# Kernel optimization log

Measured on AMD Instinct MI355X. Metric: run time of the kernel, lower is better.

Reference implementation:

```python
import jax, jax.numpy as jnp
import numpy as np

EPS = 1e-7

def setup_inputs() -> dict:
    key = jax.random.key(0)
    k1, k2, k3, k4 = jax.random.split(key, 4)
    B, F, NA = 4096, 512, 8192
    return {
        "x_real": jax.random.normal(k1, (B, F), dtype=jnp.float32),
        "x_imag": jax.random.normal(k2, (B, F), dtype=jnp.float32),
        "att_real": jax.random.normal(k3, (NA, F), dtype=jnp.float32),
        "att_imag": jax.random.normal(k4, (NA, F), dtype=jnp.float32),
        "alpha": jnp.float32(0.2),
        "top_k": 32,
    }

def _l2_normalize(v):
    # faiss.normalize_L2: divide each row by its L2 norm
    return v / jnp.linalg.norm(v, axis=1, keepdims=True)

def reference(x_real, x_imag, att_real, att_imag, alpha, top_k):
    # Database = queries themselves + attention tokens (complex, kept as re/im)
    db_re = jnp.concatenate([x_real, att_real], axis=0)   # [N, F]
    db_im = jnp.concatenate([x_imag, att_imag], axis=0)   # [N, F]
    db_reim = _l2_normalize(jnp.concatenate([db_re, db_im], axis=1))  # [N, 2F]
    q_reim = _l2_normalize(jnp.concatenate([x_real, x_imag], axis=1)) # [B, 2F]
    # IndexFlatIP on L2-normalized vectors = cosine similarity brute-force search
    sims = jnp.einsum('bd,nd->bn', q_reim, db_reim)        # [B, N]
    k = min(top_k, db_reim.shape[0])
    _, nn_idx = jax.lax.top_k(sims, k)                     # [B, K]
    nb_re = db_re[nn_idx]                                  # [B, K, F]
    nb_im = db_im[nn_idx]                                  # [B, K, F]
    # circular (polar) mean aggregation
    rho = jnp.sqrt(nb_re * nb_re + nb_im * nb_im) + EPS    # |z| + eps
    phi = jnp.arctan2(nb_im, nb_re)                        # angle(z)
    mean_rho = rho.mean(axis=1)                            # [B, F]
    mean_phi = jnp.arctan2(jnp.sin(phi).mean(axis=1), jnp.cos(phi).mean(axis=1))
    agg_re = mean_rho * jnp.cos(mean_phi)
    agg_im = mean_rho * jnp.sin(mean_phi)
    a = jnp.clip(alpha, 0.0, 1.0)
    out_re = (1.0 - a) * x_real + a * agg_re
    out_im = (1.0 - a) * x_imag + a * agg_im
    return jnp.stack([out_re, out_im], axis=0)             # [2, B, F]
```

## Files before the change

kernel.cpp:

```cpp
#include <hip/hip_runtime.h>
#include <math.h>

#define BQ   4096
#define FD   512
#define NATT 8192
#define NDB  (BQ + NATT)
#define DD   (2 * FD)
#define KTOP 32
#define EPSF 1e-7f

#define QT   32
#define NT   96
#define NTILES (2048 + 528)

typedef __attribute__((ext_vector_type(8))) short bf16x8;
typedef __attribute__((ext_vector_type(8))) unsigned short u16x8;
typedef __attribute__((ext_vector_type(4))) float f32x4;

__device__ unsigned short g_pk[(size_t)NDB * DD * 2];
__device__ float g_sims[(size_t)BQ * NDB];
__device__ float g_tmax[(size_t)BQ * NT];

__device__ __forceinline__ unsigned fkey(unsigned u) {
    return u ^ (unsigned)(((int)u >> 31) | 0x80000000);
}
__device__ __forceinline__ unsigned short f2bf(float f) {
    unsigned u = __float_as_uint(f);
    return (unsigned short)((u + 0x7FFFu + ((u >> 16) & 1u)) >> 16);
}
__device__ __forceinline__ float bf2f(unsigned short h) {
    return __uint_as_float((unsigned)h << 16);
}
__device__ __forceinline__ float frsq(float x) {
#if __has_builtin(__builtin_amdgcn_rsqf)
    return __builtin_amdgcn_rsqf(x);
#else
    return rsqrtf(x);
#endif
}
__device__ __forceinline__ void gld16(const void* g, void* l) {
    __builtin_amdgcn_global_load_lds(
        (const __attribute__((address_space(1))) void*)g,
        (__attribute__((address_space(3))) void*)l, 16, 0, 0);
}

__global__ __launch_bounds__(256) void normalize_kernel(
        const float* __restrict__ x_real, const float* __restrict__ x_imag,
        const float* __restrict__ att_real, const float* __restrict__ att_imag) {
    int t = threadIdx.x;
    int r = t >> 4;
    int l16 = t & 15;
    int row = blockIdx.x * 16 + r;
    const float *re, *im;
    if (row < BQ) { re = x_real + (size_t)row * FD;          im = x_imag + (size_t)row * FD; }
    else          { re = att_real + (size_t)(row - BQ) * FD; im = att_imag + (size_t)(row - BQ) * FD; }

    float4 vre[8], vim[8];
    float ss = 0.0f;
#pragma unroll
    for (int i = 0; i < 8; ++i) {
        vre[i] = *(const float4*)(re + l16 * 32 + i * 4);
        vim[i] = *(const float4*)(im + l16 * 32 + i * 4);
        ss += vre[i].x * vre[i].x + vre[i].y * vre[i].y + vre[i].z * vre[i].z + vre[i].w * vre[i].w;
        ss += vim[i].x * vim[i].x + vim[i].y * vim[i].y + vim[i].z * vim[i].z + vim[i].w * vim[i].w;
    }
#pragma unroll
    for (int o = 1; o < 16; o <<= 1) ss += __shfl_xor(ss, o);
    float ninv = frsq(ss);

    auto emit = [&](const float4* v, int kchunk) {
        unsigned short hi[32], lo[32];
#pragma unroll
        for (int i = 0; i < 8; ++i) {
            float vals[4] = {v[i].x, v[i].y, v[i].z, v[i].w};
#pragma unroll
            for (int j = 0; j < 4; ++j) {
                float nv = vals[j] * ninv;
                unsigned short h = f2bf(nv);
                hi[i * 4 + j] = h;
                lo[i * 4 + j] = f2bf(nv - bf2f(h));
            }
        }
        size_t cb = ((size_t)((row >> 7) * 32 + kchunk) * 2) * 4096 + (size_t)(row & 127) * 8;
#pragma unroll
        for (int kc = 0; kc < 4; ++kc) {
            *(u16x8*)(g_pk + cb + kc * 1024)        = *(u16x8*)&hi[kc * 8];
            *(u16x8*)(g_pk + cb + 4096 + kc * 1024) = *(u16x8*)&lo[kc * 8];
        }
    };
    emit(vre, l16);
    emit(vim, 16 + l16);
}

__global__ __launch_bounds__(256) void gemm_mfma() {
    __shared__ unsigned short smem[4 * 4096];
    const int t = threadIdx.x;
    const int lane = t & 63, wid = t >> 6;
    const int wr = wid >> 1, wc = wid & 1;
    const int kc = lane >> 4, fr = lane & 15;

    int tid = blockIdx.x;
    int bm, bn; bool mirror = false;
    if (tid < 2048) { bm = tid >> 6; bn = QT + (tid & 63); }
    else {
        int t2 = tid - 2048;
        int r = 0, off = 0;
        while (t2 >= off + (QT - r)) { off += QT - r; ++r; }
        bm = r; bn = r + (t2 - off);
        mirror = (bn != bm);
    }

    f32x4 acc[4][4];
#pragma unroll
    for (int m = 0; m < 4; ++m)
#pragma unroll
        for (int n = 0; n < 4; ++n) acc[m][n] = (f32x4){0.f, 0.f, 0.f, 0.f};

    for (int c = 0; c < 32; ++c) {
        const unsigned short* apk = g_pk + ((size_t)(bm * 32 + c)) * 8192;
        const unsigned short* bpk = g_pk + ((size_t)(bn * 32 + c)) * 8192;
#pragma unroll
        for (int i = 0; i < 4; ++i) {
            int s = t + i * 256;
            gld16(apk + (size_t)s * 8, &smem[s * 8]);
            gld16(bpk + (size_t)s * 8, &smem[8192 + s * 8]);
        }
        __syncthreads();

        bf16x8 ah[4], al[4], bh[4], bl[4];
#pragma unroll
        for (int m = 0; m < 4; ++m) {
            int ra = wr * 64 + m * 16 + fr;
            ah[m] = *(const bf16x8*)&smem[(kc * 128 + ra) * 8];
            al[m] = *(const bf16x8*)&smem[4096 + (kc * 128 + ra) * 8];
            int rb = wc * 64 + m * 16 + fr;
            bh[m] = *(const bf16x8*)&smem[8192 + (kc * 128 + rb) * 8];
            bl[m] = *(const bf16x8*)&smem[12288 + (kc * 128 + rb) * 8];
        }
#pragma unroll
        for (int m = 0; m < 4; ++m)
#pragma unroll
            for (int n = 0; n < 4; ++n) {
                acc[m][n] = __builtin_amdgcn_mfma_f32_16x16x32_bf16(ah[m], bh[n], acc[m][n], 0, 0, 0);
                acc[m][n] = __builtin_amdgcn_mfma_f32_16x16x32_bf16(ah[m], bl[n], acc[m][n], 0, 0, 0);
                acc[m][n] = __builtin_amdgcn_mfma_f32_16x16x32_bf16(al[m], bh[n], acc[m][n], 0, 0, 0);
            }
        __syncthreads();
    }
    const int crow0 = bm * 128 + wr * 64 + kc * 4;
    const int ccol0 = bn * 128 + wc * 64 + fr;
#pragma unroll
    for (int m = 0; m < 4; ++m)
#pragma unroll
        for (int n = 0; n < 4; ++n)
#pragma unroll
            for (int j = 0; j < 4; ++j)
                g_sims[(size_t)(crow0 + m * 16 + j) * NDB + ccol0 + n * 16] = acc[m][n][j];

    if (mirror) {
#pragma unroll
        for (int m = 0; m < 4; ++m)
#pragma unroll
            for (int n = 0; n < 4; ++n) {
                size_t r = (size_t)(bn * 128 + wc * 64 + n * 16 + fr);
                size_t cix = (size_t)(bm * 128 + wr * 64 + m * 16 + kc * 4);
                *(f32x4*)&g_sims[r * NDB + cix] = acc[m][n];
            }
    }

    float* rowhalf = (float*)smem;
    float* colhalf = (float*)smem + 256;
#pragma unroll
    for (int m = 0; m < 4; ++m)
#pragma unroll
        for (int j = 0; j < 4; ++j) {
            float v = fmaxf(fmaxf(acc[m][0][j], acc[m][1][j]),
                            fmaxf(acc[m][2][j], acc[m][3][j]));
#pragma unroll
            for (int o = 1; o < 16; o <<= 1) v = fmaxf(v, __shfl_xor(v, o));
            if (fr == 0) rowhalf[(wr * 64 + m * 16 + kc * 4 + j) * 2 + wc] = v;
        }
    if (mirror) {
#pragma unroll
        for (int n = 0; n < 4; ++n) {
            float v = acc[0][n][0];
#pragma unroll
            for (int m = 0; m < 4; ++m)
#pragma unroll
                for (int j = 0; j < 4; ++j) v = fmaxf(v, acc[m][n][j]);
            v = fmaxf(v, __shfl_xor(v, 16));
            v = fmaxf(v, __shfl_xor(v, 32));
            if (kc == 0) colhalf[(wc * 64 + n * 16 + fr) * 2 + wr] = v;
        }
    }
    __syncthreads();
    if (t < 128) {
        g_tmax[(size_t)(bm * 128 + t) * NT + bn] = fmaxf(rowhalf[t * 2], rowhalf[t * 2 + 1]);
        if (mirror)
            g_tmax[(size_t)(bn * 128 + t) * NT + bm] = fmaxf(colhalf[t * 2], colhalf[t * 2 + 1]);
    }
}

__global__ __launch_bounds__(256) void topk_agg_kernel(
        const float* __restrict__ x_real, const float* __restrict__ x_imag,
        const float* __restrict__ att_real, const float* __restrict__ att_imag,
        const float* __restrict__ alpha_p, float* __restrict__ out) {
    __shared__ float stm[96];
    __shared__ unsigned char tlist[96];
    __shared__ unsigned long long cand[512];
    __shared__ int s_idx[KTOP];
    __shared__ unsigned s_cnt;
    __shared__ int s_ntile;
    __shared__ float s_T;
    __shared__ unsigned long long s_red[4];
    __shared__ unsigned long long s_last;
    int b = blockIdx.x, t = threadIdx.x;
    int wave = t >> 6, lane = t & 63;

    if (t < 96) stm[t] = g_tmax[(size_t)b * NT + t];
    if (t == 0) { s_cnt = 0; s_ntile = 0; }
    __syncthreads();

    if (t < 96) {
        float v = stm[t];
        int cnt = 0;
        for (int i = 0; i < 96; ++i) {
            float o = stm[i];
            cnt += (o > v) || (o == v && i < t);
        }
        if (cnt == KTOP - 1) s_T = v;
    }
    __syncthreads();
    const float T = s_T;

    if (t < 96 && stm[t] >= T) {
        int p = atomicAdd(&s_ntile, 1);
        tlist[p] = (unsigned char)t;
    }
    __syncthreads();
    const int ntile = s_ntile;

    const float* rowp = g_sims + (size_t)b * NDB;
    for (int base = 0; base < ntile; base += 8) {
        int ti = base + (t >> 5);
        if (ti < ntile) {
            int tile = tlist[ti];
            int c4 = (t & 31) * 4;
            float4 v = *(const float4*)(rowp + tile * 128 + c4);
            int gidx = tile * 128 + c4;
            if (v.x >= T) { unsigned p = atomicAdd(&s_cnt, 1u); if (p < 512) cand[p] = ((unsigned long long)fkey(__float_as_uint(v.x)) << 32) | (unsigned)(~(gidx + 0)); }
            if (v.y >= T) { unsigned p = atomicAdd(&s_cnt, 1u); if (p < 512) cand[p] = ((unsigned long long)fkey(__float_as_uint(v.y)) << 32) | (unsigned)(~(gidx + 1)); }
            if (v.z >= T) { unsigned p = atomicAdd(&s_cnt, 1u); if (p < 512) cand[p] = ((unsigned long long)fkey(__float_as_uint(v.z)) << 32) | (unsigned)(~(gidx + 2)); }
            if (v.w >= T) { unsigned p = atomicAdd(&s_cnt, 1u); if (p < 512) cand[p] = ((unsigned long long)fkey(__float_as_uint(v.w)) << 32) | (unsigned)(~(gidx + 3)); }
        }
    }
    __syncthreads();

    int c = (int)s_cnt;
    if (c <= 64) {
        if (wave == 0) {
            unsigned long long vv = (lane < c) ? cand[lane] : 0ull;
#pragma unroll
            for (int k = 2; k <= 64; k <<= 1)
#pragma unroll
                for (int j = k >> 1; j > 0; j >>= 1) {
                    unsigned long long o = __shfl_xor(vv, j);
                    bool lower = (lane & j) == 0;
                    bool desc  = (lane & k) == 0;
                    bool keepmax = (lower == desc);
                    vv = keepmax ? (vv > o ? vv : o) : (vv < o ? vv : o);
                }
            if (lane < KTOP) s_idx[lane] = (int)(~(unsigned)vv);
        }
    } else if (c <= 512) {
        if (wave == 0) {
            for (int it = 0; it < KTOP; ++it) {
                unsigned long long m = 0;
                for (int i = lane; i < c; i += 64) m = cand[i] > m ? cand[i] : m;
#pragma unroll
                for (int o = 32; o > 0; o >>= 1) {
                    unsigned long long x = __shfl_xor(m, o);
                    m = x > m ? x : m;
                }
                if (lane == 0) s_idx[it] = (int)(~(unsigned)m);
                for (int i = lane; i < c; i += 64) if (cand[i] == m) cand[i] = 0;
            }
        }
    } else {
        const float4* row4 = (const float4*)rowp;
        unsigned long long last = ~0ull;
        for (int it = 0; it < KTOP; ++it) {
            unsigned long long m = 0;
            for (int i = 0; i < 12; ++i) {
                float4 v = row4[t + i * 256];
                int base = 4 * (t + i * 256);
                unsigned long long k;
                k = ((unsigned long long)fkey(__float_as_uint(v.x)) << 32) | (unsigned)(~(base + 0)); if (k < last && k > m) m = k;
                k = ((unsigned long long)fkey(__float_as_uint(v.y)) << 32) | (unsigned)(~(base + 1)); if (k < last && k > m) m = k;
                k = ((unsigned long long)fkey(__float_as_uint(v.z)) << 32) | (unsigned)(~(base + 2)); if (k < last && k > m) m = k;
                k = ((unsigned long long)fkey(__float_as_uint(v.w)) << 32) | (unsigned)(~(base + 3)); if (k < last && k > m) m = k;
            }
#pragma unroll
            for (int o = 32; o > 0; o >>= 1) {
                unsigned long long x = __shfl_xor(m, o);
                m = x > m ? x : m;
            }
            if (lane == 0) s_red[wave] = m;
            __syncthreads();
            if (t == 0) {
                unsigned long long w = s_red[0];
#pragma unroll
                for (int i = 1; i < 4; ++i) w = s_red[i] > w ? s_red[i] : w;
                s_idx[it] = (int)(~(unsigned)w);
                s_last = w;
            }
            __syncthreads();
            last = s_last;
        }
    }
    __syncthreads();

    float a = alpha_p[0];
    a = fminf(fmaxf(a, 0.0f), 1.0f);
    int f = 2 * t;
    float sr0 = 0, sc0 = 0, ss0 = 0, sr1 = 0, sc1 = 0, ss1 = 0;
    for (int k = 0; k < KTOP; ++k) {
        int idx = s_idx[k];
        const float *re, *im;
        if (idx < BQ) { re = x_real + (size_t)idx * FD;          im = x_imag + (size_t)idx * FD; }
        else          { re = att_real + (size_t)(idx - BQ) * FD; im = att_imag + (size_t)(idx - BQ) * FD; }
        float2 vr = *(const float2*)(re + f);
        float2 vi = *(const float2*)(im + f);
        float s0 = vr.x * vr.x + vi.x * vi.x;
        if (s0 > 0.0f) {
            float iv = frsq(s0);
            sr0 += s0 * iv; sc0 += vr.x * iv; ss0 += vi.x * iv;
        } else sc0 += 1.0f;
        float s1 = vr.y * vr.y + vi.y * vi.y;
        if (s1 > 0.0f) {
            float iv = frsq(s1);
            sr1 += s1 * iv; sc1 += vr.y * iv; ss1 += vi.y * iv;
        } else sc1 += 1.0f;
    }
    const float inv = 1.0f / KTOP;
    float mr0 = sr0 * inv + EPSF, mc0 = sc0 * inv, ms0 = ss0 * inv;
    float mr1 = sr1 * inv + EPSF, mc1 = sc1 * inv, ms1 = ss1 * inv;
    float q0 = mc0 * mc0 + ms0 * ms0;
    float q1 = mc1 * mc1 + ms1 * ms1;
    float i0 = (q0 > 0.0f) ? frsq(q0) : 0.0f;
    float i1 = (q1 > 0.0f) ? frsq(q1) : 0.0f;
    float c0 = (q0 > 0.0f) ? mc0 * i0 : 1.0f;
    float s0v = ms0 * i0;
    float c1 = (q1 > 0.0f) ? mc1 * i1 : 1.0f;
    float s1v = ms1 * i1;
    size_t obase = (size_t)b * FD + f;
    float2 xr = *(const float2*)(x_real + obase);
    float2 xi = *(const float2*)(x_imag + obase);
    float2 outr = make_float2((1.0f - a) * xr.x + a * (mr0 * c0),
                              (1.0f - a) * xr.y + a * (mr1 * c1));
    float2 outi = make_float2((1.0f - a) * xi.x + a * (mr0 * s0v),
                              (1.0f - a) * xi.y + a * (mr1 * s1v));
    *(float2*)(out + obase) = outr;
    *(float2*)(out + (size_t)BQ * FD + obase) = outi;
}

extern "C" void kernel_launch(void* const* d_in, const int* in_sizes, int n_in,
                              void* d_out, int out_size, void* d_ws, size_t ws_size,
                              hipStream_t stream) {
    const float* x_real   = (const float*)d_in[0];
    const float* x_imag   = (const float*)d_in[1];
    const float* att_real = (const float*)d_in[2];
    const float* att_imag = (const float*)d_in[3];
    const float* alpha    = (const float*)d_in[4];
    float* out = (float*)d_out;

    normalize_kernel<<<NDB / 16, 256, 0, stream>>>(x_real, x_imag, att_real, att_imag);
    gemm_mfma<<<NTILES, 256, 0, stream>>>();
    topk_agg_kernel<<<BQ, 256, 0, stream>>>(x_real, x_imag, att_real, att_imag, alpha, out);
}
```

Measured before the change: 376.1 us.

## Use single bf16 GEMM with fp32 rescoring of near-threshold top-k candidates

Drops the split hi/lo bf16 emulation of fp32, so the similarity GEMM runs one MFMA per tile pair instead of three and loads half the packed data. To keep top-k selection exact, the selection threshold is widened by a margin. Candidates whose bf16 score falls inside that ambiguity band are rescored in fp32 against the original inputs using stored inverse norms. If too many candidates sit near the boundary, a fallback path rescores every candidate. This adds candidate-handling complexity and depends on the margin bounding the bf16 error.

New measurement: 333.0 us. 11.5% less time.

```diff
diff --git a/kernel.cpp b/kernel.cpp
--- a/kernel.cpp
+++ b/kernel.cpp
@@ -8,6 +8,7 @@
 #define DD   (2 * FD)
 #define KTOP 32
 #define EPSF 1e-7f
+#define DEL2 0.004f
 
 #define QT   32
 #define NT   96
@@ -17,19 +18,21 @@
 typedef __attribute__((ext_vector_type(8))) unsigned short u16x8;
 typedef __attribute__((ext_vector_type(4))) float f32x4;
 
-__device__ unsigned short g_pk[(size_t)NDB * DD * 2];
+__device__ unsigned short g_pk[(size_t)NDB * DD];
 __device__ float g_sims[(size_t)BQ * NDB];
 __device__ float g_tmax[(size_t)BQ * NT];
+__device__ float g_ninv[NDB];
 
 __device__ __forceinline__ unsigned fkey(unsigned u) {
     return u ^ (unsigned)(((int)u >> 31) | 0x80000000);
+}
+__device__ __forceinline__ float unfkey(unsigned fk) {
+    unsigned u = (fk & 0x80000000u) ? (fk ^ 0x80000000u) : ~fk;
+    return __uint_as_float(u);
 }
 __device__ __forceinline__ unsigned short f2bf(float f) {
     unsigned u = __float_as_uint(f);
     return (unsigned short)((u + 0x7FFFu + ((u >> 16) & 1u)) >> 16);
-}
-__device__ __forceinline__ float bf2f(unsigned short h) {
-    return __uint_as_float((unsigned)h << 16);
 }
 __device__ __forceinline__ float frsq(float x) {
 #if __has_builtin(__builtin_amdgcn_rsqf)
@@ -67,33 +70,27 @@
 #pragma unroll
     for (int o = 1; o < 16; o <<= 1) ss += __shfl_xor(ss, o);
     float ninv = frsq(ss);
+    if (l16 == 0) g_ninv[row] = ninv;
 
     auto emit = [&](const float4* v, int kchunk) {
-        unsigned short hi[32], lo[32];
+        unsigned short hi[32];
 #pragma unroll
         for (int i = 0; i < 8; ++i) {
             float vals[4] = {v[i].x, v[i].y, v[i].z, v[i].w};
 #pragma unroll
-            for (int j = 0; j < 4; ++j) {
-                float nv = vals[j] * ninv;
-                unsigned short h = f2bf(nv);
-                hi[i * 4 + j] = h;
-                lo[i * 4 + j] = f2bf(nv - bf2f(h));
-            }
-        }
-        size_t cb = ((size_t)((row >> 7) * 32 + kchunk) * 2) * 4096 + (size_t)(row & 127) * 8;
-#pragma unroll
-        for (int kc = 0; kc < 4; ++kc) {
-            *(u16x8*)(g_pk + cb + kc * 1024)        = *(u16x8*)&hi[kc * 8];
-            *(u16x8*)(g_pk + cb + 4096 + kc * 1024) = *(u16x8*)&lo[kc * 8];
-        }
+            for (int j = 0; j < 4; ++j) hi[i * 4 + j] = f2bf(vals[j] * ninv);
+        }
+        size_t cb = ((size_t)((row >> 7) * 32 + kchunk)) * 4096 + (size_t)(row & 127) * 8;
+#pragma unroll
+        for (int kc = 0; kc < 4; ++kc)
+            *(u16x8*)(g_pk + cb + kc * 1024) = *(u16x8*)&hi[kc * 8];
     };
     emit(vre, l16);
     emit(vim, 16 + l16);
 }
 
 __global__ __launch_bounds__(256) void gemm_mfma() {
-    __shared__ unsigned short smem[4 * 4096];
+    __shared__ unsigned short smem[2 * 4096];
     const int t = threadIdx.x;
     const int lane = t & 63, wid = t >> 6;
     const int wr = wid >> 1, wc = wid & 1;
@@ -117,34 +114,29 @@
         for (int n = 0; n < 4; ++n) acc[m][n] = (f32x4){0.f, 0.f, 0.f, 0.f};
 
     for (int c = 0; c < 32; ++c) {
-        const unsigned short* apk = g_pk + ((size_t)(bm * 32 + c)) * 8192;
-        const unsigned short* bpk = g_pk + ((size_t)(bn * 32 + c)) * 8192;
-#pragma unroll
-        for (int i = 0; i < 4; ++i) {
+        const unsigned short* apk = g_pk + ((size_t)(bm * 32 + c)) * 4096;
+        const unsigned short* bpk = g_pk + ((size_t)(bn * 32 + c)) * 4096;
+#pragma unroll
+        for (int i = 0; i < 2; ++i) {
             int s = t + i * 256;
             gld16(apk + (size_t)s * 8, &smem[s * 8]);
-            gld16(bpk + (size_t)s * 8, &smem[8192 + s * 8]);
-        }
-        __syncthreads();
-
-        bf16x8 ah[4], al[4], bh[4], bl[4];
+            gld16(bpk + (size_t)s * 8, &smem[4096 + s * 8]);
+        }
+        __syncthreads();
+
+        bf16x8 ah[4], bh[4];
 #pragma unroll
         for (int m = 0; m < 4; ++m) {
             int ra = wr * 64 + m * 16 + fr;
             ah[m] = *(const bf16x8*)&smem[(kc * 128 + ra) * 8];
-            al[m] = *(const bf16x8*)&smem[4096 + (kc * 128 + ra) * 8];
             int rb = wc * 64 + m * 16 + fr;
-            bh[m] = *(const bf16x8*)&smem[8192 + (kc * 128 + rb) * 8];
-            bl[m] = *(const bf16x8*)&smem[12288 + (kc * 128 + rb) * 8];
+            bh[m] = *(const bf16x8*)&smem[4096 + (kc * 128 + rb) * 8];
         }
 #pragma unroll
         for (int m = 0; m < 4; ++m)
 #pragma unroll
-            for (int n = 0; n < 4; ++n) {
+            for (int n = 0; n < 4; ++n)
                 acc[m][n] = __builtin_amdgcn_mfma_f32_16x16x32_bf16(ah[m], bh[n], acc[m][n], 0, 0, 0);
-                acc[m][n] = __builtin_amdgcn_mfma_f32_16x16x32_bf16(ah[m], bl[n], acc[m][n], 0, 0, 0);
-                acc[m][n] = __builtin_amdgcn_mfma_f32_16x16x32_bf16(al[m], bh[n], acc[m][n], 0, 0, 0);
-            }
         __syncthreads();
     }
     const int crow0 = bm * 128 + wr * 64 + kc * 4;
@@ -207,18 +199,24 @@
         const float* __restrict__ alpha_p, float* __restrict__ out) {
     __shared__ float stm[96];
     __shared__ unsigned char tlist[96];
-    __shared__ unsigned long long cand[512];
+    __shared__ unsigned long long cand[1024];
+    __shared__ unsigned long long skey[64];
+    __shared__ unsigned long long rkey[64];
+    __shared__ int ridx[64];
     __shared__ int s_idx[KTOP];
+    __shared__ float qre[FD], qim[FD];
     __shared__ unsigned s_cnt;
-    __shared__ int s_ntile;
-    __shared__ float s_T;
+    __shared__ int s_ntile, s_S, s_R;
+    __shared__ float s_T, s_V32;
     __shared__ unsigned long long s_red[4];
     __shared__ unsigned long long s_last;
     int b = blockIdx.x, t = threadIdx.x;
     int wave = t >> 6, lane = t & 63;
 
     if (t < 96) stm[t] = g_tmax[(size_t)b * NT + t];
-    if (t == 0) { s_cnt = 0; s_ntile = 0; }
+    if (t < 128) *(float4*)&qre[t * 4] = *(const float4*)(x_real + (size_t)b * FD + t * 4);
+    else         *(float4*)&qim[(t - 128) * 4] = *(const float4*)(x_imag + (size_t)b * FD + (t - 128) * 4);
+    if (t == 0) { s_cnt = 0; s_ntile = 0; s_S = 0; s_R = 0; }
     __syncthreads();
 
     if (t < 96) {
@@ -231,12 +229,9 @@
         if (cnt == KTOP - 1) s_T = v;
     }
     __syncthreads();
-    const float T = s_T;
-
-    if (t < 96 && stm[t] >= T) {
-        int p = atomicAdd(&s_ntile, 1);
-        tlist[p] = (unsigned char)t;
-    }
+    const float Tm = s_T - DEL2;
+
+    if (t < 96 && stm[t] >= Tm) { int p = atomicAdd(&s_ntile, 1); tlist[p] = (unsigned char)t; }
     __syncthreads();
     const int ntile = s_ntile;
 
@@ -248,15 +243,16 @@
             int c4 = (t & 31) * 4;
             float4 v = *(const float4*)(rowp + tile * 128 + c4);
             int gidx = tile * 128 + c4;
-            if (v.x >= T) { unsigned p = atomicAdd(&s_cnt, 1u); if (p < 512) cand[p] = ((unsigned long long)fkey(__float_as_uint(v.x)) << 32) | (unsigned)(~(gidx + 0)); }
-            if (v.y >= T) { unsigned p = atomicAdd(&s_cnt, 1u); if (p < 512) cand[p] = ((unsigned long long)fkey(__float_as_uint(v.y)) << 32) | (unsigned)(~(gidx + 1)); }
-            if (v.z >= T) { unsigned p = atomicAdd(&s_cnt, 1u); if (p < 512) cand[p] = ((unsigned long long)fkey(__float_as_uint(v.z)) << 32) | (unsigned)(~(gidx + 2)); }
-            if (v.w >= T) { unsigned p = atomicAdd(&s_cnt, 1u); if (p < 512) cand[p] = ((unsigned long long)fkey(__float_as_uint(v.w)) << 32) | (unsigned)(~(gidx + 3)); }
-        }
-    }
-    __syncthreads();
-
-    int c = (int)s_cnt;
+            if (v.x >= Tm) { unsigned p = atomicAdd(&s_cnt, 1u); if (p < 1024) cand[p] = ((unsigned long long)fkey(__float_as_uint(v.x)) << 32) | (unsigned)(~(gidx + 0)); }
+            if (v.y >= Tm) { unsigned p = atomicAdd(&s_cnt, 1u); if (p < 1024) cand[p] = ((unsigned long long)fkey(__float_as_uint(v.y)) << 32) | (unsigned)(~(gidx + 1)); }
+            if (v.z >= Tm) { unsigned p = atomicAdd(&s_cnt, 1u); if (p < 1024) cand[p] = ((unsigned long long)fkey(__float_as_uint(v.z)) << 32) | (unsigned)(~(gidx + 2)); }
+            if (v.w >= Tm) { unsigned p = atomicAdd(&s_cnt, 1u); if (p < 1024) cand[p] = ((unsigned long long)fkey(__float_as_uint(v.w)) << 32) | (unsigned)(~(gidx + 3)); }
+        }
+    }
+    __syncthreads();
+    unsigned cnt_raw = s_cnt;
+    int c = (int)cnt_raw; if (c > 1024) c = 1024;
+
     if (c <= 64) {
         if (wave == 0) {
             unsigned long long vv = (lane < c) ? cand[lane] : 0ull;
@@ -270,49 +266,122 @@
                     bool keepmax = (lower == desc);
                     vv = keepmax ? (vv > o ? vv : o) : (vv < o ? vv : o);
                 }
-            if (lane < KTOP) s_idx[lane] = (int)(~(unsigned)vv);
-        }
-    } else if (c <= 512) {
-        if (wave == 0) {
-            for (int it = 0; it < KTOP; ++it) {
-                unsigned long long m = 0;
-                for (int i = lane; i < c; i += 64) m = cand[i] > m ? cand[i] : m;
-#pragma unroll
-                for (int o = 32; o > 0; o >>= 1) {
-                    unsigned long long x = __shfl_xor(m, o);
-                    m = x > m ? x : m;
-                }
-                if (lane == 0) s_idx[it] = (int)(~(unsigned)m);
-                for (int i = lane; i < c; i += 64) if (cand[i] == m) cand[i] = 0;
-            }
-        }
+            skey[lane] = vv;
+        }
+        __syncthreads();
     } else {
-        const float4* row4 = (const float4*)rowp;
         unsigned long long last = ~0ull;
-        for (int it = 0; it < KTOP; ++it) {
+        for (int it = 0; it < 64; ++it) {
             unsigned long long m = 0;
-            for (int i = 0; i < 12; ++i) {
-                float4 v = row4[t + i * 256];
-                int base = 4 * (t + i * 256);
-                unsigned long long k;
-                k = ((unsigned long long)fkey(__float_as_uint(v.x)) << 32) | (unsigned)(~(base + 0)); if (k < last && k > m) m = k;
-                k = ((unsigned long long)fkey(__float_as_uint(v.y)) << 32) | (unsigned)(~(base + 1)); if (k < last && k > m) m = k;
-                k = ((unsigned long long)fkey(__float_as_uint(v.z)) << 32) | (unsigned)(~(base + 2)); if (k < last && k > m) m = k;
-                k = ((unsigned long long)fkey(__float_as_uint(v.w)) << 32) | (unsigned)(~(base + 3)); if (k < last && k > m) m = k;
-            }
-#pragma unroll
-            for (int o = 32; o > 0; o >>= 1) {
-                unsigned long long x = __shfl_xor(m, o);
-                m = x > m ? x : m;
-            }
+            for (int i = t; i < c; i += 256) { unsigned long long k = cand[i]; if (k < last && k > m) m = k; }
+#pragma unroll
+            for (int o = 32; o > 0; o >>= 1) { unsigned long long x = __shfl_xor(m, o); m = x > m ? x : m; }
             if (lane == 0) s_red[wave] = m;
             __syncthreads();
             if (t == 0) {
                 unsigned long long w = s_red[0];
 #pragma unroll
                 for (int i = 1; i < 4; ++i) w = s_red[i] > w ? s_red[i] : w;
-                s_idx[it] = (int)(~(unsigned)w);
-                s_last = w;
+                skey[it] = w; s_last = w;
+            }
+            __syncthreads();
+            last = s_last;
+        }
+    }
+    if (t == 0) s_V32 = unfkey((unsigned)(skey[31] >> 32));
+    __syncthreads();
+    const float V32 = s_V32;
+    bool fallback = (cnt_raw > 1024);
+    if (c > 64) {
+        float v63 = unfkey((unsigned)(skey[63] >> 32));
+        fallback = fallback || (v63 >= V32 - DEL2);
+    }
+    const float qninv = g_ninv[b];
+
+    if (!fallback) {
+        if (wave == 0) {
+            unsigned long long k = skey[lane];
+            float v = (k != 0) ? unfkey((unsigned)(k >> 32)) : -INFINITY;
+            int idx = (int)(~(unsigned)k);
+            bool sure = v > V32 + DEL2;
+            bool amb  = !sure && v >= V32 - DEL2;
+            unsigned long long smask = __ballot(sure);
+            int S = __popcll(smask);
+            if (sure) s_idx[lane] = idx;
+            if (amb)  ridx[lane - S] = idx;
+            if (lane == 0) { s_S = S; }
+            unsigned long long amask = __ballot(amb);
+            if (lane == 0) { s_R = __popcll(amask); }
+        }
+        __syncthreads();
+        int S = s_S, R = s_R;
+        for (int r = wave; r < R; r += 4) {
+            int j = ridx[r];
+            const float *dre, *dim_;
+            if (j < BQ) { dre = x_real + (size_t)j * FD; dim_ = x_imag + (size_t)j * FD; }
+            else        { dre = att_real + (size_t)(j - BQ) * FD; dim_ = att_imag + (size_t)(j - BQ) * FD; }
+            float4 a0 = *(const float4*)&qre[lane * 8], a1 = *(const float4*)&qre[lane * 8 + 4];
+            float4 b0 = *(const float4*)(dre + lane * 8), b1 = *(const float4*)(dre + lane * 8 + 4);
+            float4 c0 = *(const float4*)&qim[lane * 8], c1 = *(const float4*)&qim[lane * 8 + 4];
+            float4 d0 = *(const float4*)(dim_ + lane * 8), d1 = *(const float4*)(dim_ + lane * 8 + 4);
+            float s = a0.x * b0.x + a0.y * b0.y + a0.z * b0.z + a0.w * b0.w
+                    + a1.x * b1.x + a1.y * b1.y + a1.z * b1.z + a1.w * b1.w
+                    + c0.x * d0.x + c0.y * d0.y + c0.z * d0.z + c0.w * d0.w
+                    + c1.x * d1.x + c1.y * d1.y + c1.z * d1.z + c1.w * d1.w;
+#pragma unroll
+            for (int o = 32; o > 0; o >>= 1) s += __shfl_xor(s, o);
+            float v = s * qninv * g_ninv[j];
+            if (lane == 0) rkey[r] = ((unsigned long long)fkey(__float_as_uint(v)) << 32) | (unsigned)(~j);
+        }
+        __syncthreads();
+        if (wave == 0) {
+            unsigned long long vv = (lane < R) ? rkey[lane] : 0ull;
+#pragma unroll
+            for (int k = 2; k <= 64; k <<= 1)
+#pragma unroll
+                for (int j = k >> 1; j > 0; j >>= 1) {
+                    unsigned long long o = __shfl_xor(vv, j);
+                    bool lower = (lane & j) == 0;
+                    bool desc  = (lane & k) == 0;
+                    bool keepmax = (lower == desc);
+                    vv = keepmax ? (vv > o ? vv : o) : (vv < o ? vv : o);
+                }
+            if (lane < KTOP - S) s_idx[S + lane] = (int)(~(unsigned)vv);
+        }
+        __syncthreads();
+    } else {
+        for (int r = wave; r < c; r += 4) {
+            int j = (int)(~(unsigned)cand[r]);
+            const float *dre, *dim_;
+            if (j < BQ) { dre = x_real + (size_t)j * FD; dim_ = x_imag + (size_t)j * FD; }
+            else        { dre = att_real + (size_t)(j - BQ) * FD; dim_ = att_imag + (size_t)(j - BQ) * FD; }
+            float4 a0 = *(const float4*)&qre[lane * 8], a1 = *(const float4*)&qre[lane * 8 + 4];
+            float4 b0 = *(const float4*)(dre + lane * 8), b1 = *(const float4*)(dre + lane * 8 + 4);
+            float4 c0 = *(const float4*)&qim[lane * 8], c1 = *(const float4*)&qim[lane * 8 + 4];
+            float4 d0 = *(const float4*)(dim_ + lane * 8), d1 = *(const float4*)(dim_ + lane * 8 + 4);
+            float s = a0.x * b0.x + a0.y * b0.y + a0.z * b0.z + a0.w * b0.w
+                    + a1.x * b1.x + a1.y * b1.y + a1.z * b1.z + a1.w * b1.w
+                    + c0.x * d0.x + c0.y * d0.y + c0.z * d0.z + c0.w * d0.w
+                    + c1.x * d1.x + c1.y * d1.y + c1.z * d1.z + c1.w * d1.w;
+#pragma unroll
+            for (int o = 32; o > 0; o >>= 1) s += __shfl_xor(s, o);
+            float v = s * qninv * g_ninv[j];
+            if (lane == 0) cand[r] = ((unsigned long long)fkey(__float_as_uint(v)) << 32) | (unsigned)(~j);
+        }
+        __syncthreads();
+        unsigned long long last = ~0ull;
+        for (int it = 0; it < KTOP; ++it) {
+            unsigned long long m = 0;
+            for (int i = t; i < c; i += 256) { unsigned long long k = cand[i]; if (k < last && k > m) m = k; }
+#pragma unroll
+            for (int o = 32; o > 0; o >>= 1) { unsigned long long x = __shfl_xor(m, o); m = x > m ? x : m; }
+            if (lane == 0) s_red[wave] = m;
+            __syncthreads();
+            if (t == 0) {
+                unsigned long long w = s_red[0];
+#pragma unroll
+                for (int i = 1; i < 4; ++i) w = s_red[i] > w ? s_red[i] : w;
+                s_idx[it] = (int)(~(unsigned)w); s_last = w;
             }
             __syncthreads();
             last = s_last;
@@ -349,15 +418,15 @@
     float q1 = mc1 * mc1 + ms1 * ms1;
     float i0 = (q0 > 0.0f) ? frsq(q0) : 0.0f;
     float i1 = (q1 > 0.0f) ? frsq(q1) : 0.0f;
-    float c0 = (q0 > 0.0f) ? mc0 * i0 : 1.0f;
+    float c0v = (q0 > 0.0f) ? mc0 * i0 : 1.0f;
     float s0v = ms0 * i0;
-    float c1 = (q1 > 0.0f) ? mc1 * i1 : 1.0f;
+    float c1v = (q1 > 0.0f) ? mc1 * i1 : 1.0f;
     float s1v = ms1 * i1;
     size_t obase = (size_t)b * FD + f;
     float2 xr = *(const float2*)(x_real + obase);
     float2 xi = *(const float2*)(x_imag + obase);
-    float2 outr = make_float2((1.0f - a) * xr.x + a * (mr0 * c0),
-                              (1.0f - a) * xr.y + a * (mr1 * c1));
+    float2 outr = make_float2((1.0f - a) * xr.x + a * (mr0 * c0v),
+                              (1.0f - a) * xr.y + a * (mr1 * c1v));
     float2 outi = make_float2((1.0f - a) * xi.x + a * (mr0 * s0v),
                               (1.0f - a) * xi.y + a * (mr1 * s1v));
     *(float2*)(out + obase) = outr;
```
